# Performance work log

Measured on AMD Instinct MI355X. Metric: run time of the kernel, lower is better.

## Reference

```python
import jax, jax.numpy as jnp
import numpy as np

N_NODES = 100000
N_EDGES = 1000000
IN_DIM = 128
HID1 = 64
HID2 = 64
OUT_DIM = 1
NUM_GRAPHS = 2048


def setup_inputs() -> dict:
    key = jax.random.key(0)
    ks = jax.random.split(key, 12)
    x = jax.random.normal(ks[0], (N_NODES, IN_DIM), dtype=jnp.float32)
    edge_index = jax.random.randint(ks[1], (2, N_EDGES), 0, N_NODES, dtype=jnp.int64)
    batch = jnp.sort(jax.random.randint(ks[2], (N_NODES,), 0, NUM_GRAPHS, dtype=jnp.int64))
    s1 = 1.0 / np.sqrt(IN_DIM)
    s2 = 1.0 / np.sqrt(HID1)
    s3 = 1.0 / np.sqrt(HID2)
    return {
        "x": x,
        "edge_index": edge_index,
        "batch": batch,
        "W1": jax.random.normal(ks[3], (IN_DIM, HID1), dtype=jnp.float32) * s1,
        "b1": jnp.zeros((HID1,), dtype=jnp.float32),
        "W2": jax.random.normal(ks[4], (HID1, HID2), dtype=jnp.float32) * s2,
        "b2": jnp.zeros((HID2,), dtype=jnp.float32),
        "attn_w": jax.random.normal(ks[5], (HID2, 1), dtype=jnp.float32) * s3,
        "attn_b": jnp.zeros((1,), dtype=jnp.float32),
        "mask_w": jax.random.normal(ks[6], (HID2, 1), dtype=jnp.float32) * s3,
        "mask_b": jnp.zeros((1,), dtype=jnp.float32),
        "out_w": jax.random.normal(ks[7], (HID2, OUT_DIM), dtype=jnp.float32) * s3,
        "out_b": jnp.zeros((OUT_DIM,), dtype=jnp.float32),
    }


def reference(x, edge_index, batch, W1, b1, W2, b2, attn_w, attn_b, mask_w, mask_b, out_w, out_b):
    n = x.shape[0]
    # GCNConv (PyG default): add self-loops, symmetric normalization
    loop = jnp.arange(n, dtype=edge_index.dtype)
    row = jnp.concatenate([edge_index[0], loop])  # source nodes
    col = jnp.concatenate([edge_index[1], loop])  # target nodes
    deg = jax.ops.segment_sum(jnp.ones_like(col, dtype=x.dtype), col, num_segments=n)
    dinv = jnp.where(deg > 0, jax.lax.rsqrt(jnp.maximum(deg, 1e-12)), 0.0)
    norm = dinv[row] * dinv[col]  # [E+N]

    def conv(h, W, b):
        h = h @ W                              # [N, out]
        m = h[row] * norm[:, None]             # gather + scale  [E+N, out]
        return jax.ops.segment_sum(m, col, num_segments=n) + b

    h = jax.nn.relu(conv(x, W1, b1))
    h = jax.nn.relu(conv(h, W2, b2))
    # AttentionPooling: (attn score * sigmoid mask)-weighted scatter-sum per graph
    scores = (h @ attn_w + attn_b) * jax.nn.sigmoid(h @ mask_w + mask_b)  # [N,1]
    pooled = jax.ops.segment_sum(h * scores, batch, num_segments=NUM_GRAPHS)  # [G, HID2]
    return pooled @ out_w + out_b
```

## Files before the change

kernel.cpp:

```cpp
#include <hip/hip_runtime.h>
#include <math.h>


#define NB 64
#define SEG 16
#define CAPS 80
#define SLOTS (SEG * CAPS)
#define BIN_BLOCKS 256

__global__ __launch_bounds__(256) void gemm_bin_kernel(
    const float* __restrict__ X, const float* __restrict__ W,
    float* __restrict__ P, int N, int K,
    const int* __restrict__ row, const int* __restrict__ col,
    int* __restrict__ bcnt, int* __restrict__ gbuf, int E,
    float* __restrict__ out, const float* __restrict__ out_b, int G) {
    __shared__ float Wl[32 * 64];
    __shared__ float xs[128 * 33];

    if (blockIdx.x < BIN_BLOCKS) {
        int seg = blockIdx.x & (SEG - 1);
        int t = blockIdx.x * 256 + threadIdx.x;
        if (t < G) out[t] = out_b[0];
        for (int e = t; e < E; e += BIN_BLOCKS * 256) {
            int c = col[e];
            int b = c >> 6;
            int pos = atomicAdd(&bcnt[(b * SEG + seg) * 16], 1);
            if (pos < CAPS) gbuf[b * SLOTS + seg * CAPS + pos] = row[e] | ((c & 63) << 17);
        }
        return;
    }

    const int tid = threadIdx.x;
    const int cg = tid & 3;
    const int ng = tid >> 2;
    const int node0 = (blockIdx.x - BIN_BLOCKS) * 128;

    float acc[2][16];
#pragma unroll
    for (int r = 0; r < 2; r++)
#pragma unroll
        for (int j = 0; j < 16; j++) acc[r][j] = 0.0f;

    for (int k0 = 0; k0 < K; k0 += 32) {
        const float4* Wg = (const float4*)(W + (size_t)k0 * 64);
#pragma unroll
        for (int f = tid; f < 512; f += 256) ((float4*)Wl)[f] = Wg[f];
        {
            int rrow = tid >> 1;
            int q0 = (tid & 1) * 16;
            int node = node0 + rrow;
            const float* Xr = X + (size_t)node * K + k0 + q0;
            float* xd = &xs[rrow * 33 + q0];
#pragma unroll
            for (int q = 0; q < 4; q++) {
                float4 v = make_float4(0.f, 0.f, 0.f, 0.f);
                if (node < N) v = *(const float4*)(Xr + 4 * q);
                xd[4 * q + 0] = v.x;
                xd[4 * q + 1] = v.y;
                xd[4 * q + 2] = v.z;
                xd[4 * q + 3] = v.w;
            }
        }
        __syncthreads();
#pragma unroll
        for (int kk = 0; kk < 32; kk++) {
            float xv0 = xs[(ng * 2 + 0) * 33 + kk];
            float xv1 = xs[(ng * 2 + 1) * 33 + kk];
            const float* wr = &Wl[kk * 64 + cg * 4];
            float4 w0 = *(const float4*)(wr + 0);
            float4 w1 = *(const float4*)(wr + 16);
            float4 w2 = *(const float4*)(wr + 32);
            float4 w3 = *(const float4*)(wr + 48);
#pragma unroll
            for (int r = 0; r < 2; r++) {
                float xv = r ? xv1 : xv0;
                acc[r][0]  = fmaf(xv, w0.x, acc[r][0]);
                acc[r][1]  = fmaf(xv, w0.y, acc[r][1]);
                acc[r][2]  = fmaf(xv, w0.z, acc[r][2]);
                acc[r][3]  = fmaf(xv, w0.w, acc[r][3]);
                acc[r][4]  = fmaf(xv, w1.x, acc[r][4]);
                acc[r][5]  = fmaf(xv, w1.y, acc[r][5]);
                acc[r][6]  = fmaf(xv, w1.z, acc[r][6]);
                acc[r][7]  = fmaf(xv, w1.w, acc[r][7]);
                acc[r][8]  = fmaf(xv, w2.x, acc[r][8]);
                acc[r][9]  = fmaf(xv, w2.y, acc[r][9]);
                acc[r][10] = fmaf(xv, w2.z, acc[r][10]);
                acc[r][11] = fmaf(xv, w2.w, acc[r][11]);
                acc[r][12] = fmaf(xv, w3.x, acc[r][12]);
                acc[r][13] = fmaf(xv, w3.y, acc[r][13]);
                acc[r][14] = fmaf(xv, w3.z, acc[r][14]);
                acc[r][15] = fmaf(xv, w3.w, acc[r][15]);
            }
        }
        __syncthreads();
    }

#pragma unroll
    for (int r = 0; r < 2; r++) {
        int node = node0 + ng * 2 + r;
        if (node < N) {
            float* dst = P + (size_t)node * 64 + cg * 4;
#pragma unroll
            for (int m = 0; m < 4; m++) {
                float4 v = make_float4(acc[r][4 * m + 0], acc[r][4 * m + 1],
                                       acc[r][4 * m + 2], acc[r][4 * m + 3]);
                *(float4*)(dst + 16 * m) = v;
            }
        }
    }
}

__global__ __launch_bounds__(256) void sort_kernel(
    const int* __restrict__ bcnt, const int* __restrict__ gbuf,
    int* __restrict__ csr, int* __restrict__ startcnt,
    float* __restrict__ dinv, int N) {
    __shared__ int scnt[SEG], segoff[SEG], s_tot;
    __shared__ int ebuf[SLOTS];
    __shared__ int lcnt[NB], lcur[NB];
    const int tid = threadIdx.x;
    const int b = blockIdx.x;
    const int base = b * SLOTS;

    if (tid < SEG) {
        int c = bcnt[(b * SEG + tid) * 16];
        scnt[tid] = c < CAPS ? c : CAPS;
    }
    if (tid < NB) lcnt[tid] = 0;
    __syncthreads();
    if (tid == 0) {
        int o = 0;
        for (int s = 0; s < SEG; s++) { segoff[s] = o; o += scnt[s]; }
        s_tot = o;
    }
    __syncthreads();
    for (int idx = tid; idx < SLOTS; idx += 256) {
        int seg = idx / CAPS;
        int j = idx - seg * CAPS;
        if (j < scnt[seg]) {
            int w = gbuf[base + idx];
            ebuf[segoff[seg] + j] = w;
            atomicAdd(&lcnt[(w >> 17) & 63], 1);
        }
    }
    __syncthreads();
    if (tid < NB) {
        int cntv = lcnt[tid];
        int rnd = (cntv + 3) & ~3;
        int val = rnd;
#pragma unroll
        for (int off = 1; off < 64; off <<= 1) {
            int n = __shfl_up(val, off, 64);
            if (tid >= off) val += n;
        }
        int st = val - rnd;
        lcur[tid] = st;
        int v = b * NB + tid;
        if (v < N) {
            dinv[v] = rsqrtf(1.0f + (float)cntv);
            int cc = cntv < 127 ? cntv : 127;
            startcnt[v] = ((base + st) << 7) | cc;
        }
    }
    __syncthreads();
    int tot = s_tot;
    for (int idx = tid; idx < tot; idx += 256) {
        int w = ebuf[idx];
        int vl = (w >> 17) & 63;
        int pp = atomicAdd(&lcur[vl], 1);
        csr[base + pp] = w & 131071;
    }
}

__global__ __launch_bounds__(256) void gather_gemm_kernel(
    const float* __restrict__ P, const int* __restrict__ csr,
    const int* __restrict__ startcnt, const float* __restrict__ dinv,
    const float* __restrict__ b1, const float* __restrict__ W2,
    float* __restrict__ Q, int N) {
    __shared__ float hs[64 * 65];
    __shared__ float Wl[64 * 64];
    const int tid = threadIdx.x;
    const int v0 = blockIdx.x * 64;
    const int vend = (v0 + 64 < N) ? v0 + 64 : N;
    const int p = tid & 15;
    const int p4 = p * 4;

    for (int f = tid; f < 1024; f += 256)
        ((float4*)Wl)[f] = ((const float4*)W2)[f];

    const float4 bb = ((const float4*)b1)[p];
    for (int v = v0 + (tid >> 4); v < vend; v += 16) {
        int pack = startcnt[v];
        int st = pack >> 7;
        int c = pack & 127;
        float dv = dinv[v];
        float4 a0 = *(const float4*)(P + (size_t)v * 64 + p4);
        float4 acc = make_float4(a0.x * dv, a0.y * dv, a0.z * dv, a0.w * dv);
        for (int i = 0; i < c; i += 8) {
            int4 ua = *(const int4*)(csr + st + i);
            int4 ub = *(const int4*)(csr + st + i + 4);
            float du0 = dinv[ua.x], du1 = dinv[ua.y], du2 = dinv[ua.z], du3 = dinv[ua.w];
            float du4 = dinv[ub.x], du5 = dinv[ub.y], du6 = dinv[ub.z], du7 = dinv[ub.w];
            float4 m0 = *(const float4*)(P + (size_t)ua.x * 64 + p4);
            float4 m1 = *(const float4*)(P + (size_t)ua.y * 64 + p4);
            float4 m2 = *(const float4*)(P + (size_t)ua.z * 64 + p4);
            float4 m3 = *(const float4*)(P + (size_t)ua.w * 64 + p4);
            float4 m4 = *(const float4*)(P + (size_t)ub.x * 64 + p4);
            float4 m5 = *(const float4*)(P + (size_t)ub.y * 64 + p4);
            float4 m6 = *(const float4*)(P + (size_t)ub.z * 64 + p4);
            float4 m7 = *(const float4*)(P + (size_t)ub.w * 64 + p4);
            acc.x = fmaf(m0.x, du0, acc.x); acc.y = fmaf(m0.y, du0, acc.y);
            acc.z = fmaf(m0.z, du0, acc.z); acc.w = fmaf(m0.w, du0, acc.w);
            if (i + 1 < c) { acc.x = fmaf(m1.x, du1, acc.x); acc.y = fmaf(m1.y, du1, acc.y);
                             acc.z = fmaf(m1.z, du1, acc.z); acc.w = fmaf(m1.w, du1, acc.w); }
            if (i + 2 < c) { acc.x = fmaf(m2.x, du2, acc.x); acc.y = fmaf(m2.y, du2, acc.y);
                             acc.z = fmaf(m2.z, du2, acc.z); acc.w = fmaf(m2.w, du2, acc.w); }
            if (i + 3 < c) { acc.x = fmaf(m3.x, du3, acc.x); acc.y = fmaf(m3.y, du3, acc.y);
                             acc.z = fmaf(m3.z, du3, acc.z); acc.w = fmaf(m3.w, du3, acc.w); }
            if (i + 4 < c) { acc.x = fmaf(m4.x, du4, acc.x); acc.y = fmaf(m4.y, du4, acc.y);
                             acc.z = fmaf(m4.z, du4, acc.z); acc.w = fmaf(m4.w, du4, acc.w); }
            if (i + 5 < c) { acc.x = fmaf(m5.x, du5, acc.x); acc.y = fmaf(m5.y, du5, acc.y);
                             acc.z = fmaf(m5.z, du5, acc.z); acc.w = fmaf(m5.w, du5, acc.w); }
            if (i + 6 < c) { acc.x = fmaf(m6.x, du6, acc.x); acc.y = fmaf(m6.y, du6, acc.y);
                             acc.z = fmaf(m6.z, du6, acc.z); acc.w = fmaf(m6.w, du6, acc.w); }
            if (i + 7 < c) { acc.x = fmaf(m7.x, du7, acc.x); acc.y = fmaf(m7.y, du7, acc.y);
                             acc.z = fmaf(m7.z, du7, acc.z); acc.w = fmaf(m7.w, du7, acc.w); }
        }
        float* hd = &hs[(v - v0) * 65 + p4];
        hd[0] = fmaxf(fmaf(acc.x, dv, bb.x), 0.f);
        hd[1] = fmaxf(fmaf(acc.y, dv, bb.y), 0.f);
        hd[2] = fmaxf(fmaf(acc.z, dv, bb.z), 0.f);
        hd[3] = fmaxf(fmaf(acc.w, dv, bb.w), 0.f);
    }
    __syncthreads();

    const int cg = tid & 3;
    const int n0 = tid >> 2;
    float acc[16];
#pragma unroll
    for (int j = 0; j < 16; j++) acc[j] = 0.0f;
    for (int kk = 0; kk < 64; kk++) {
        float xv = hs[n0 * 65 + kk];
        const float* wr = &Wl[kk * 64 + cg * 4];
        float4 w0 = *(const float4*)(wr + 0);
        float4 w1 = *(const float4*)(wr + 16);
        float4 w2 = *(const float4*)(wr + 32);
        float4 w3 = *(const float4*)(wr + 48);
        acc[0]  = fmaf(xv, w0.x, acc[0]);
        acc[1]  = fmaf(xv, w0.y, acc[1]);
        acc[2]  = fmaf(xv, w0.z, acc[2]);
        acc[3]  = fmaf(xv, w0.w, acc[3]);
        acc[4]  = fmaf(xv, w1.x, acc[4]);
        acc[5]  = fmaf(xv, w1.y, acc[5]);
        acc[6]  = fmaf(xv, w1.z, acc[6]);
        acc[7]  = fmaf(xv, w1.w, acc[7]);
        acc[8]  = fmaf(xv, w2.x, acc[8]);
        acc[9]  = fmaf(xv, w2.y, acc[9]);
        acc[10] = fmaf(xv, w2.z, acc[10]);
        acc[11] = fmaf(xv, w2.w, acc[11]);
        acc[12] = fmaf(xv, w3.x, acc[12]);
        acc[13] = fmaf(xv, w3.y, acc[13]);
        acc[14] = fmaf(xv, w3.z, acc[14]);
        acc[15] = fmaf(xv, w3.w, acc[15]);
    }
    int node = v0 + n0;
    if (node < N) {
        float d = dinv[node];
        float* dst = Q + (size_t)node * 64 + cg * 4;
        for (int m = 0; m < 4; m++) {
            float4 v = make_float4(acc[4 * m + 0] * d, acc[4 * m + 1] * d,
                                   acc[4 * m + 2] * d, acc[4 * m + 3] * d);
            *(float4*)(dst + 16 * m) = v;
        }
    }
}

#define GP_NODES 64
__global__ __launch_bounds__(256) void gather_pool_kernel(
    const float* __restrict__ Q, const int* __restrict__ csr,
    const int* __restrict__ startcnt, const float* __restrict__ dinv,
    const float* __restrict__ bias, const int* __restrict__ batch,
    const float* __restrict__ attn_w, const float* __restrict__ attn_b,
    const float* __restrict__ mask_w, const float* __restrict__ mask_b,
    const float* __restrict__ out_w, float* __restrict__ out, int N) {
    __shared__ float pacc[2048];
    __shared__ int s_gmin, s_span;
    const int tid = threadIdx.x;
    const int v0 = blockIdx.x * GP_NODES;
    const int vend = (v0 + GP_NODES < N) ? v0 + GP_NODES : N;
    if (tid == 0) {
        int gmin = batch[v0];
        s_gmin = gmin;
        s_span = batch[vend - 1] - gmin + 1;
    }
    __syncthreads();
    const int gmin = s_gmin, span = s_span;
    for (int i = tid; i < span; i += 256) pacc[i] = 0.f;
    __syncthreads();

    const int p = tid & 15;
    const int p4 = p * 4;
    const float4 wa = ((const float4*)attn_w)[p];
    const float4 wm = ((const float4*)mask_w)[p];
    const float4 wo = ((const float4*)out_w)[p];
    const float4 bb = ((const float4*)bias)[p];
    const float ab = attn_b[0], mb = mask_b[0];

    for (int v = v0 + (tid >> 4); v < vend; v += 16) {
        int pack = startcnt[v];
        int st = pack >> 7;
        int c = pack & 127;
        float dv = dinv[v];
        float4 acc = *(const float4*)(Q + (size_t)v * 64 + p4);
        for (int i = 0; i < c; i += 8) {
            int4 ua = *(const int4*)(csr + st + i);
            int4 ub = *(const int4*)(csr + st + i + 4);
            float4 m0 = *(const float4*)(Q + (size_t)ua.x * 64 + p4);
            float4 m1 = *(const float4*)(Q + (size_t)ua.y * 64 + p4);
            float4 m2 = *(const float4*)(Q + (size_t)ua.z * 64 + p4);
            float4 m3 = *(const float4*)(Q + (size_t)ua.w * 64 + p4);
            float4 m4 = *(const float4*)(Q + (size_t)ub.x * 64 + p4);
            float4 m5 = *(const float4*)(Q + (size_t)ub.y * 64 + p4);
            float4 m6 = *(const float4*)(Q + (size_t)ub.z * 64 + p4);
            float4 m7 = *(const float4*)(Q + (size_t)ub.w * 64 + p4);
            acc.x += m0.x; acc.y += m0.y; acc.z += m0.z; acc.w += m0.w;
            if (i + 1 < c) { acc.x += m1.x; acc.y += m1.y; acc.z += m1.z; acc.w += m1.w; }
            if (i + 2 < c) { acc.x += m2.x; acc.y += m2.y; acc.z += m2.z; acc.w += m2.w; }
            if (i + 3 < c) { acc.x += m3.x; acc.y += m3.y; acc.z += m3.z; acc.w += m3.w; }
            if (i + 4 < c) { acc.x += m4.x; acc.y += m4.y; acc.z += m4.z; acc.w += m4.w; }
            if (i + 5 < c) { acc.x += m5.x; acc.y += m5.y; acc.z += m5.z; acc.w += m5.w; }
            if (i + 6 < c) { acc.x += m6.x; acc.y += m6.y; acc.z += m6.z; acc.w += m6.w; }
            if (i + 7 < c) { acc.x += m7.x; acc.y += m7.y; acc.z += m7.z; acc.w += m7.w; }
        }
        float hx = fmaxf(fmaf(acc.x, dv, bb.x), 0.f);
        float hy = fmaxf(fmaf(acc.y, dv, bb.y), 0.f);
        float hz = fmaxf(fmaf(acc.z, dv, bb.z), 0.f);
        float hw = fmaxf(fmaf(acc.w, dv, bb.w), 0.f);
        float pa = hx * wa.x + hy * wa.y + hz * wa.z + hw * wa.w;
        float pm = hx * wm.x + hy * wm.y + hz * wm.z + hw * wm.w;
        float po = hx * wo.x + hy * wo.y + hz * wo.z + hw * wo.w;
#pragma unroll
        for (int off = 1; off < 16; off <<= 1) {
            pa += __shfl_xor(pa, off, 64);
            pm += __shfl_xor(pm, off, 64);
            po += __shfl_xor(po, off, 64);
        }
        if (p == 0) {
            float cc = (pa + ab) * (1.0f / (1.0f + expf(-(pm + mb)))) * po;
            atomicAdd(&pacc[batch[v] - gmin], cc);
        }
    }
    __syncthreads();
    for (int i = tid; i < span; i += 256) {
        float val = pacc[i];
        if (val != 0.f) atomicAdd(&out[gmin + i], val);
    }
}

extern "C" void kernel_launch(void* const* d_in, const int* in_sizes, int n_in,
                              void* d_out, int out_size, void* d_ws, size_t ws_size,
                              hipStream_t stream) {
    const float* x      = (const float*)d_in[0];
    const int*   edge   = (const int*)d_in[1];
    const int*   batch  = (const int*)d_in[2];
    const float* W1     = (const float*)d_in[3];
    const float* b1     = (const float*)d_in[4];
    const float* W2     = (const float*)d_in[5];
    const float* b2     = (const float*)d_in[6];
    const float* attn_w = (const float*)d_in[7];
    const float* attn_b = (const float*)d_in[8];
    const float* mask_w = (const float*)d_in[9];
    const float* mask_b = (const float*)d_in[10];
    const float* out_w  = (const float*)d_in[11];
    const float* out_b  = (const float*)d_in[12];
    float* out = (float*)d_out;

    const int N  = in_sizes[2];
    const int E  = in_sizes[1] / 2;
    const int K1 = in_sizes[0] / N;
    const int H  = in_sizes[4];
    const int G  = out_size;
    const int* row = edge;
    const int* col = edge + E;

    const int NBUCK = (N + NB - 1) / NB;

    char* ws = (char*)d_ws;
    auto align256 = [](size_t s) { return (s + 255) / 256 * 256; };
    int*   bcnt     = (int*)ws;   ws += align256((size_t)NBUCK * SEG * 16 * 4);
    int*   gbuf     = (int*)ws;   ws += align256((size_t)NBUCK * SLOTS * 4);
    int*   csr      = (int*)ws;   ws += align256((size_t)NBUCK * SLOTS * 4);
    int*   startcnt = (int*)ws;   ws += align256((size_t)N * 4);
    float* dinv     = (float*)ws; ws += align256((size_t)N * 4);
    float* P        = (float*)ws; ws += align256((size_t)N * H * 4);
    float* Q        = (float*)ws;

    const int gblocks = (N + 127) / 128;

    hipMemsetAsync(bcnt, 0, (size_t)NBUCK * SEG * 16 * 4, stream);
    hipMemsetAsync(csr, 0, (size_t)NBUCK * SLOTS * 4, stream);

    gemm_bin_kernel<<<BIN_BLOCKS + gblocks, 256, 0, stream>>>(
        x, W1, P, N, K1, row, col, bcnt, gbuf, E, out, out_b, G);

    sort_kernel<<<NBUCK, 256, 0, stream>>>(bcnt, gbuf, csr, startcnt, dinv, N);

    gather_gemm_kernel<<<NBUCK, 256, 0, stream>>>(
        P, csr, startcnt, dinv, b1, W2, Q, N);

    gather_pool_kernel<<<NBUCK, 256, 0, stream>>>(
        Q, csr, startcnt, dinv, b2, batch, attn_w, attn_b, mask_w, mask_b, out_w, out, N);
}
```

Before: 278.2 us.

## Prescale P by source dinv in sort kernel and retile both GEMMs

The layer-1 features P are now multiplied by each node's dinv inside the sort kernel, right after the degrees are known. The layer-1 gather can then plain-add neighbor rows and skip the eight random dinv loads per chunk. Separately, the first GEMM now stores X transposed in shared memory so one float4 read feeds 4 nodes × 8 columns per thread, and the second GEMM computes 2 nodes × 8 columns per thread. The cost is an extra read-modify-write pass over P in the sort kernel, plus different register and LDS access patterns.

```diff
diff --git a/kernel.cpp b/kernel.cpp
--- a/kernel.cpp
+++ b/kernel.cpp
@@ -15,7 +15,7 @@
     int* __restrict__ bcnt, int* __restrict__ gbuf, int E,
     float* __restrict__ out, const float* __restrict__ out_b, int G) {
     __shared__ float Wl[32 * 64];
-    __shared__ float xs[128 * 33];
+    __shared__ float xs[32 * 132];
 
     if (blockIdx.x < BIN_BLOCKS) {
         int seg = blockIdx.x & (SEG - 1);
@@ -31,15 +31,15 @@
     }
 
     const int tid = threadIdx.x;
-    const int cg = tid & 3;
-    const int ng = tid >> 2;
+    const int cg = tid & 7;
+    const int ng = tid >> 3;
     const int node0 = (blockIdx.x - BIN_BLOCKS) * 128;
 
-    float acc[2][16];
-#pragma unroll
-    for (int r = 0; r < 2; r++)
-#pragma unroll
-        for (int j = 0; j < 16; j++) acc[r][j] = 0.0f;
+    float acc[4][8];
+#pragma unroll
+    for (int r = 0; r < 4; r++)
+#pragma unroll
+        for (int j = 0; j < 8; j++) acc[r][j] = 0.0f;
 
     for (int k0 = 0; k0 < K; k0 += 32) {
         const float4* Wg = (const float4*)(W + (size_t)k0 * 64);
@@ -50,62 +50,47 @@
             int q0 = (tid & 1) * 16;
             int node = node0 + rrow;
             const float* Xr = X + (size_t)node * K + k0 + q0;
-            float* xd = &xs[rrow * 33 + q0];
 #pragma unroll
             for (int q = 0; q < 4; q++) {
                 float4 v = make_float4(0.f, 0.f, 0.f, 0.f);
                 if (node < N) v = *(const float4*)(Xr + 4 * q);
-                xd[4 * q + 0] = v.x;
-                xd[4 * q + 1] = v.y;
-                xd[4 * q + 2] = v.z;
-                xd[4 * q + 3] = v.w;
+                int kb = q0 + 4 * q;
+                xs[(kb + 0) * 132 + rrow] = v.x;
+                xs[(kb + 1) * 132 + rrow] = v.y;
+                xs[(kb + 2) * 132 + rrow] = v.z;
+                xs[(kb + 3) * 132 + rrow] = v.w;
             }
         }
         __syncthreads();
 #pragma unroll
         for (int kk = 0; kk < 32; kk++) {
-            float xv0 = xs[(ng * 2 + 0) * 33 + kk];
-            float xv1 = xs[(ng * 2 + 1) * 33 + kk];
-            const float* wr = &Wl[kk * 64 + cg * 4];
+            float4 xv = *(const float4*)&xs[kk * 132 + ng * 4];
+            const float* wr = &Wl[kk * 64 + cg * 8];
             float4 w0 = *(const float4*)(wr + 0);
-            float4 w1 = *(const float4*)(wr + 16);
-            float4 w2 = *(const float4*)(wr + 32);
-            float4 w3 = *(const float4*)(wr + 48);
-#pragma unroll
-            for (int r = 0; r < 2; r++) {
-                float xv = r ? xv1 : xv0;
-                acc[r][0]  = fmaf(xv, w0.x, acc[r][0]);
-                acc[r][1]  = fmaf(xv, w0.y, acc[r][1]);
-                acc[r][2]  = fmaf(xv, w0.z, acc[r][2]);
-                acc[r][3]  = fmaf(xv, w0.w, acc[r][3]);
-                acc[r][4]  = fmaf(xv, w1.x, acc[r][4]);
-                acc[r][5]  = fmaf(xv, w1.y, acc[r][5]);
-                acc[r][6]  = fmaf(xv, w1.z, acc[r][6]);
-                acc[r][7]  = fmaf(xv, w1.w, acc[r][7]);
-                acc[r][8]  = fmaf(xv, w2.x, acc[r][8]);
-                acc[r][9]  = fmaf(xv, w2.y, acc[r][9]);
-                acc[r][10] = fmaf(xv, w2.z, acc[r][10]);
-                acc[r][11] = fmaf(xv, w2.w, acc[r][11]);
-                acc[r][12] = fmaf(xv, w3.x, acc[r][12]);
-                acc[r][13] = fmaf(xv, w3.y, acc[r][13]);
-                acc[r][14] = fmaf(xv, w3.z, acc[r][14]);
-                acc[r][15] = fmaf(xv, w3.w, acc[r][15]);
+            float4 w1 = *(const float4*)(wr + 4);
+#pragma unroll
+            for (int r = 0; r < 4; r++) {
+                float xr = (r == 0) ? xv.x : (r == 1) ? xv.y : (r == 2) ? xv.z : xv.w;
+                acc[r][0] = fmaf(xr, w0.x, acc[r][0]);
+                acc[r][1] = fmaf(xr, w0.y, acc[r][1]);
+                acc[r][2] = fmaf(xr, w0.z, acc[r][2]);
+                acc[r][3] = fmaf(xr, w0.w, acc[r][3]);
+                acc[r][4] = fmaf(xr, w1.x, acc[r][4]);
+                acc[r][5] = fmaf(xr, w1.y, acc[r][5]);
+                acc[r][6] = fmaf(xr, w1.z, acc[r][6]);
+                acc[r][7] = fmaf(xr, w1.w, acc[r][7]);
             }
         }
         __syncthreads();
     }
 
 #pragma unroll
-    for (int r = 0; r < 2; r++) {
-        int node = node0 + ng * 2 + r;
+    for (int r = 0; r < 4; r++) {
+        int node = node0 + ng * 4 + r;
         if (node < N) {
-            float* dst = P + (size_t)node * 64 + cg * 4;
-#pragma unroll
-            for (int m = 0; m < 4; m++) {
-                float4 v = make_float4(acc[r][4 * m + 0], acc[r][4 * m + 1],
-                                       acc[r][4 * m + 2], acc[r][4 * m + 3]);
-                *(float4*)(dst + 16 * m) = v;
-            }
+            float* dst = P + (size_t)node * 64 + cg * 8;
+            *(float4*)(dst + 0) = make_float4(acc[r][0], acc[r][1], acc[r][2], acc[r][3]);
+            *(float4*)(dst + 4) = make_float4(acc[r][4], acc[r][5], acc[r][6], acc[r][7]);
         }
     }
 }
@@ -113,10 +98,11 @@
 __global__ __launch_bounds__(256) void sort_kernel(
     const int* __restrict__ bcnt, const int* __restrict__ gbuf,
     int* __restrict__ csr, int* __restrict__ startcnt,
-    float* __restrict__ dinv, int N) {
+    float* __restrict__ dinv, float* __restrict__ P, int N) {
     __shared__ int scnt[SEG], segoff[SEG], s_tot;
     __shared__ int ebuf[SLOTS];
     __shared__ int lcnt[NB], lcur[NB];
+    __shared__ float sdinv[NB];
     const int tid = threadIdx.x;
     const int b = blockIdx.x;
     const int base = b * SLOTS;
@@ -154,9 +140,11 @@
         }
         int st = val - rnd;
         lcur[tid] = st;
+        float d = rsqrtf(1.0f + (float)cntv);
+        sdinv[tid] = d;
         int v = b * NB + tid;
         if (v < N) {
-            dinv[v] = rsqrtf(1.0f + (float)cntv);
+            dinv[v] = d;
             int cc = cntv < 127 ? cntv : 127;
             startcnt[v] = ((base + st) << 7) | cc;
         }
@@ -168,6 +156,17 @@
         int vl = (w >> 17) & 63;
         int pp = atomicAdd(&lcur[vl], 1);
         csr[base + pp] = w & 131071;
+    }
+    for (int idx = tid; idx < NB * 16; idx += 256) {
+        int r = idx >> 4;
+        int v = b * NB + r;
+        if (v < N) {
+            float d = sdinv[r];
+            float4* pp = (float4*)(P + (size_t)v * 64) + (idx & 15);
+            float4 t = *pp;
+            t.x *= d; t.y *= d; t.z *= d; t.w *= d;
+            *pp = t;
+        }
     }
 }
 
@@ -193,13 +192,10 @@
         int st = pack >> 7;
         int c = pack & 127;
         float dv = dinv[v];
-        float4 a0 = *(const float4*)(P + (size_t)v * 64 + p4);
-        float4 acc = make_float4(a0.x * dv, a0.y * dv, a0.z * dv, a0.w * dv);
+        float4 acc = *(const float4*)(P + (size_t)v * 64 + p4);
         for (int i = 0; i < c; i += 8) {
             int4 ua = *(const int4*)(csr + st + i);
             int4 ub = *(const int4*)(csr + st + i + 4);
-            float du0 = dinv[ua.x], du1 = dinv[ua.y], du2 = dinv[ua.z], du3 = dinv[ua.w];
-            float du4 = dinv[ub.x], du5 = dinv[ub.y], du6 = dinv[ub.z], du7 = dinv[ub.w];
             float4 m0 = *(const float4*)(P + (size_t)ua.x * 64 + p4);
             float4 m1 = *(const float4*)(P + (size_t)ua.y * 64 + p4);
             float4 m2 = *(const float4*)(P + (size_t)ua.z * 64 + p4);
@@ -208,22 +204,14 @@
             float4 m5 = *(const float4*)(P + (size_t)ub.y * 64 + p4);
             float4 m6 = *(const float4*)(P + (size_t)ub.z * 64 + p4);
             float4 m7 = *(const float4*)(P + (size_t)ub.w * 64 + p4);
-            acc.x = fmaf(m0.x, du0, acc.x); acc.y = fmaf(m0.y, du0, acc.y);
-            acc.z = fmaf(m0.z, du0, acc.z); acc.w = fmaf(m0.w, du0, acc.w);
-            if (i + 1 < c) { acc.x = fmaf(m1.x, du1, acc.x); acc.y = fmaf(m1.y, du1, acc.y);
-                             acc.z = fmaf(m1.z, du1, acc.z); acc.w = fmaf(m1.w, du1, acc.w); }
-            if (i + 2 < c) { acc.x = fmaf(m2.x, du2, acc.x); acc.y = fmaf(m2.y, du2, acc.y);
-                             acc.z = fmaf(m2.z, du2, acc.z); acc.w = fmaf(m2.w, du2, acc.w); }
-            if (i + 3 < c) { acc.x = fmaf(m3.x, du3, acc.x); acc.y = fmaf(m3.y, du3, acc.y);
-                             acc.z = fmaf(m3.z, du3, acc.z); acc.w = fmaf(m3.w, du3, acc.w); }
-            if (i + 4 < c) { acc.x = fmaf(m4.x, du4, acc.x); acc.y = fmaf(m4.y, du4, acc.y);
-                             acc.z = fmaf(m4.z, du4, acc.z); acc.w = fmaf(m4.w, du4, acc.w); }
-            if (i + 5 < c) { acc.x = fmaf(m5.x, du5, acc.x); acc.y = fmaf(m5.y, du5, acc.y);
-                             acc.z = fmaf(m5.z, du5, acc.z); acc.w = fmaf(m5.w, du5, acc.w); }
-            if (i + 6 < c) { acc.x = fmaf(m6.x, du6, acc.x); acc.y = fmaf(m6.y, du6, acc.y);
-                             acc.z = fmaf(m6.z, du6, acc.z); acc.w = fmaf(m6.w, du6, acc.w); }
-            if (i + 7 < c) { acc.x = fmaf(m7.x, du7, acc.x); acc.y = fmaf(m7.y, du7, acc.y);
-                             acc.z = fmaf(m7.z, du7, acc.z); acc.w = fmaf(m7.w, du7, acc.w); }
+            acc.x += m0.x; acc.y += m0.y; acc.z += m0.z; acc.w += m0.w;
+            if (i + 1 < c) { acc.x += m1.x; acc.y += m1.y; acc.z += m1.z; acc.w += m1.w; }
+            if (i + 2 < c) { acc.x += m2.x; acc.y += m2.y; acc.z += m2.z; acc.w += m2.w; }
+            if (i + 3 < c) { acc.x += m3.x; acc.y += m3.y; acc.z += m3.z; acc.w += m3.w; }
+            if (i + 4 < c) { acc.x += m4.x; acc.y += m4.y; acc.z += m4.z; acc.w += m4.w; }
+            if (i + 5 < c) { acc.x += m5.x; acc.y += m5.y; acc.z += m5.z; acc.w += m5.w; }
+            if (i + 6 < c) { acc.x += m6.x; acc.y += m6.y; acc.z += m6.z; acc.w += m6.w; }
+            if (i + 7 < c) { acc.x += m7.x; acc.y += m7.y; acc.z += m7.z; acc.w += m7.w; }
         }
         float* hd = &hs[(v - v0) * 65 + p4];
         hd[0] = fmaxf(fmaf(acc.x, dv, bb.x), 0.f);
@@ -233,43 +221,46 @@
     }
     __syncthreads();
 
-    const int cg = tid & 3;
-    const int n0 = tid >> 2;
-    float acc[16];
-#pragma unroll
-    for (int j = 0; j < 16; j++) acc[j] = 0.0f;
+    const int cg = tid & 7;
+    const int n0 = tid >> 3;
+    float acc2[2][8];
+#pragma unroll
+    for (int r = 0; r < 2; r++)
+#pragma unroll
+        for (int j = 0; j < 8; j++) acc2[r][j] = 0.0f;
     for (int kk = 0; kk < 64; kk++) {
-        float xv = hs[n0 * 65 + kk];
-        const float* wr = &Wl[kk * 64 + cg * 4];
+        float x0 = hs[(n0 * 2 + 0) * 65 + kk];
+        float x1 = hs[(n0 * 2 + 1) * 65 + kk];
+        const float* wr = &Wl[kk * 64 + cg * 8];
         float4 w0 = *(const float4*)(wr + 0);
-        float4 w1 = *(const float4*)(wr + 16);
-        float4 w2 = *(const float4*)(wr + 32);
-        float4 w3 = *(const float4*)(wr + 48);
-        acc[0]  = fmaf(xv, w0.x, acc[0]);
-        acc[1]  = fmaf(xv, w0.y, acc[1]);
-        acc[2]  = fmaf(xv, w0.z, acc[2]);
-        acc[3]  = fmaf(xv, w0.w, acc[3]);
-        acc[4]  = fmaf(xv, w1.x, acc[4]);
-        acc[5]  = fmaf(xv, w1.y, acc[5]);
-        acc[6]  = fmaf(xv, w1.z, acc[6]);
-        acc[7]  = fmaf(xv, w1.w, acc[7]);
-        acc[8]  = fmaf(xv, w2.x, acc[8]);
-        acc[9]  = fmaf(xv, w2.y, acc[9]);
-        acc[10] = fmaf(xv, w2.z, acc[10]);
-        acc[11] = fmaf(xv, w2.w, acc[11]);
-        acc[12] = fmaf(xv, w3.x, acc[12]);
-        acc[13] = fmaf(xv, w3.y, acc[13]);
-        acc[14] = fmaf(xv, w3.z, acc[14]);
-        acc[15] = fmaf(xv, w3.w, acc[15]);
-    }
-    int node = v0 + n0;
-    if (node < N) {
-        float d = dinv[node];
-        float* dst = Q + (size_t)node * 64 + cg * 4;
-        for (int m = 0; m < 4; m++) {
-            float4 v = make_float4(acc[4 * m + 0] * d, acc[4 * m + 1] * d,
-                                   acc[4 * m + 2] * d, acc[4 * m + 3] * d);
-            *(float4*)(dst + 16 * m) = v;
+        float4 w1 = *(const float4*)(wr + 4);
+        acc2[0][0] = fmaf(x0, w0.x, acc2[0][0]);
+        acc2[0][1] = fmaf(x0, w0.y, acc2[0][1]);
+        acc2[0][2] = fmaf(x0, w0.z, acc2[0][2]);
+        acc2[0][3] = fmaf(x0, w0.w, acc2[0][3]);
+        acc2[0][4] = fmaf(x0, w1.x, acc2[0][4]);
+        acc2[0][5] = fmaf(x0, w1.y, acc2[0][5]);
+        acc2[0][6] = fmaf(x0, w1.z, acc2[0][6]);
+        acc2[0][7] = fmaf(x0, w1.w, acc2[0][7]);
+        acc2[1][0] = fmaf(x1, w0.x, acc2[1][0]);
+        acc2[1][1] = fmaf(x1, w0.y, acc2[1][1]);
+        acc2[1][2] = fmaf(x1, w0.z, acc2[1][2]);
+        acc2[1][3] = fmaf(x1, w0.w, acc2[1][3]);
+        acc2[1][4] = fmaf(x1, w1.x, acc2[1][4]);
+        acc2[1][5] = fmaf(x1, w1.y, acc2[1][5]);
+        acc2[1][6] = fmaf(x1, w1.z, acc2[1][6]);
+        acc2[1][7] = fmaf(x1, w1.w, acc2[1][7]);
+    }
+#pragma unroll
+    for (int r = 0; r < 2; r++) {
+        int node = v0 + n0 * 2 + r;
+        if (node < N) {
+            float d = dinv[node];
+            float* dst = Q + (size_t)node * 64 + cg * 8;
+            *(float4*)(dst + 0) = make_float4(acc2[r][0] * d, acc2[r][1] * d,
+                                              acc2[r][2] * d, acc2[r][3] * d);
+            *(float4*)(dst + 4) = make_float4(acc2[r][4] * d, acc2[r][5] * d,
+                                              acc2[r][6] * d, acc2[r][7] * d);
         }
     }
 }
@@ -402,7 +393,7 @@
     gemm_bin_kernel<<<BIN_BLOCKS + gblocks, 256, 0, stream>>>(
         x, W1, P, N, K1, row, col, bcnt, gbuf, E, out, out_b, G);
 
-    sort_kernel<<<NBUCK, 256, 0, stream>>>(bcnt, gbuf, csr, startcnt, dinv, N);
+    sort_kernel<<<NBUCK, 256, 0, stream>>>(bcnt, gbuf, csr, startcnt, dinv, P, N);
 
     gather_gemm_kernel<<<NBUCK, 256, 0, stream>>>(
         P, csr, startcnt, dinv, b1, W2, Q, N);
```

Result: no change. 279.6 us (+0.5%).
